# Kernel tuning notes

Measured on AMD Instinct MI355X. Metric: run time of the kernel, lower is better.

Reference implementation:

```python
import jax, jax.numpy as jnp
import numpy as np

K = 7          # involution kernel size
GC = 16        # group_channels (hardcoded in module)
BN_EPS = 1e-5
LN_EPS = 1e-6


def _forward(x, conv1_w, conv1_b, bn_gamma, bn_beta, bn_mean, bn_var,
             conv2_w, conv2_b, ln_w, ln_b, w1, b1, w2, b2):
    b, c, h, w = x.shape
    groups = c // GC
    # --- involution: dynamic kernel generation (1x1 conv -> BN(eval) -> ReLU -> 1x1 conv) ---
    t = jnp.einsum('bchw,oc->bohw', x, conv1_w) + conv1_b[None, :, None, None]
    t = (t - bn_mean[None, :, None, None]) * (bn_gamma / jnp.sqrt(bn_var + BN_EPS))[None, :, None, None] \
        + bn_beta[None, :, None, None]
    t = jax.nn.relu(t)
    wgt = jnp.einsum('bchw,oc->bohw', t, conv2_w) + conv2_b[None, :, None, None]
    wgt = wgt.reshape(b, groups, K * K, h, w)                  # (b,g,k2,h,w)
    # --- unfold: gather kxk neighborhoods (channel-major, then kh, kw — matches torch Unfold) ---
    p = (K - 1) // 2
    xp = jnp.pad(x, ((0, 0), (0, 0), (p, p), (p, p)))
    patches = jnp.stack([xp[:, :, i:i + h, j:j + w]
                         for i in range(K) for j in range(K)], axis=2)   # (b,c,k2,h,w)
    patches = patches.reshape(b, groups, GC, K * K, h, w)
    # weighted sum over kernel positions
    out = jnp.einsum('bgkhw,bgckhw->bgchw', wgt, patches).reshape(b, c, h, w)
    # --- LN + MLP residual (channels_last) ---
    y = out.transpose(0, 2, 3, 1)                               # (b,h,w,c)
    mu = y.mean(-1, keepdims=True)
    var = ((y - mu) ** 2).mean(-1, keepdims=True)
    y = (y - mu) / jnp.sqrt(var + LN_EPS) * ln_w + ln_b
    y = jax.nn.gelu(y @ w1.T + b1, approximate=False)           # torch GELU = exact erf
    y = y @ w2.T + b2                                           # dropout_rate=0 -> identity
    return y.transpose(0, 3, 1, 2) + x


def setup_inputs() -> dict:
    key = jax.random.key(0)
    ks = jax.random.split(key, 6)
    dim = 128
    groups = dim // GC
    red = dim // 4
    b, h, w = 8, 56, 56
    return {
        'x': jax.random.normal(ks[0], (b, dim, h, w), jnp.float32),
        'conv1_w': jax.random.normal(ks[1], (red, dim), jnp.float32) * (1.0 / np.sqrt(dim)),
        'conv1_b': jnp.zeros((red,), jnp.float32),
        'bn_gamma': jnp.ones((red,), jnp.float32),
        'bn_beta': jnp.zeros((red,), jnp.float32),
        'bn_mean': jnp.zeros((red,), jnp.float32),
        'bn_var': jnp.ones((red,), jnp.float32),
        'conv2_w': jax.random.normal(ks[2], (K * K * groups, red), jnp.float32) * (1.0 / np.sqrt(red)),
        'conv2_b': jnp.zeros((K * K * groups,), jnp.float32),
        'ln_w': jnp.ones((dim,), jnp.float32),
        'ln_b': jnp.zeros((dim,), jnp.float32),
        'w1': jax.random.normal(ks[3], (4 * dim, dim), jnp.float32) * (1.0 / np.sqrt(dim)),
        'b1': jnp.zeros((4 * dim,), jnp.float32),
        'w2': jax.random.normal(ks[4], (dim, 4 * dim), jnp.float32) * (1.0 / np.sqrt(4 * dim)),
        'b2': jnp.zeros((dim,), jnp.float32),
    }


def reference(x, conv1_w, conv1_b, bn_gamma, bn_beta, bn_mean, bn_var,
              conv2_w, conv2_b, ln_w, ln_b, w1, b1, w2, b2):
    return _forward(x, conv1_w, conv1_b, bn_gamma, bn_beta, bn_mean, bn_var,
                    conv2_w, conv2_b, ln_w, ln_b, w1, b1, w2, b2)
```

## Files before the change

### kernel.cpp

```cpp
#include <hip/hip_runtime.h>
#include <hip/hip_bf16.h>
#include <math.h>

#define HW    3136
#define WIMG  56
#define NPIX  25088
#define CIN   128
#define RED   32
#define NGROUP 8
#define GCH   16
#define KKK   49

typedef __attribute__((ext_vector_type(8))) short short8;
typedef __attribute__((ext_vector_type(4))) float f32x4;
typedef unsigned short ushort_t;

static __device__ __forceinline__ unsigned int f2b(float f) {
    union { __hip_bfloat16 b; unsigned short u; } cv;
    cv.b = __float2bfloat16(f);
    return (unsigned int)cv.u;
}

static __device__ __forceinline__ float gelu_t(float h) {
    float z = h * fmaf(0.0356774081f, h * h, 0.7978845608f);
    float e = __expf(-2.f * z);
    return __fdividef(h, 1.f + e);
}

__global__ __launch_bounds__(256) void k_prep(const float* __restrict__ conv1_w,
    const float* __restrict__ conv1_b, const float* __restrict__ bn_g,
    const float* __restrict__ bn_b, const float* __restrict__ bn_m,
    const float* __restrict__ bn_v, const float* __restrict__ conv2_w,
    const float* __restrict__ ln_w, const float* __restrict__ w1,
    const float* __restrict__ w2,
    ushort_t* __restrict__ c1b, ushort_t* __restrict__ c2b,
    ushort_t* __restrict__ lw1b, ushort_t* __restrict__ w2b,
    float* __restrict__ sc1, float* __restrict__ sh1)
{
    int id = blockIdx.x * 256 + threadIdx.x;
    w2b[id] = (ushort_t)f2b(w2[id]);
    int c = id & 127;
    lw1b[id] = (ushort_t)f2b(w1[id] * ln_w[c]);
    if (id < 4096)  c1b[id] = (ushort_t)f2b(conv1_w[id]);
    if (id < 12800) c2b[id] = (id < 12544) ? (ushort_t)f2b(conv2_w[id]) : (ushort_t)0;
    if (id < 32) {
        float sc = bn_g[id] * rsqrtf(bn_v[id] + 1e-5f);
        sc1[id] = sc;
        sh1[id] = (conv1_b[id] - bn_m[id]) * sc + bn_b[id];
    }
}

__global__ void k_prep2(const float* __restrict__ w1, const float* __restrict__ ln_w,
    const float* __restrict__ ln_b, const float* __restrict__ b1,
    float* __restrict__ s1, float* __restrict__ t1)
{
    int n = threadIdx.x;
    const float* wr = w1 + (size_t)n * 128;
    float s = 0.f, t = 0.f;
    #pragma unroll 8
    for (int c = 0; c < 128; ++c) { float w = wr[c]; s += ln_w[c] * w; t += ln_b[c] * w; }
    s1[n] = s; t1[n] = t + b1[n];
}

__global__ __launch_bounds__(256) void k_mega(const float* __restrict__ x,
    const short* __restrict__ c1b, const short* __restrict__ c2b,
    const float* __restrict__ sc1, const float* __restrict__ sh1,
    const float* __restrict__ c2bias,
    const ushort_t* __restrict__ lw1b, const ushort_t* __restrict__ w2b,
    const float* __restrict__ s1, const float* __restrict__ t1,
    const float* __restrict__ b2, float* __restrict__ outp)
{
    __shared__ __align__(16) char smem[79936];
    short* swg  = (short*)smem;
    short* sh   = (short*)smem;
    short* sx   = (short*)smem + 26656;
    short* st   = (short*)(smem + 70720);
    float* sred  = (float*)(smem + 70720);
    float* sred2 = sred + 1088;
    float* smu   = sred2 + 1088;
    float* srs   = smu + 64;

    int tid  = threadIdx.x;
    int P0   = blockIdx.x * 64;
    int b    = P0 / HW;
    int p0i  = P0 - b * HW;
    int lane = tid & 63, wv = tid >> 6;
    int ln15 = lane & 15, quad = lane >> 4;

    const float* xb = x + (size_t)b * CIN * HW + p0i;
    #pragma unroll
    for (int it = 0; it < 32; ++it) {
        int idx = it * 256 + tid;
        int c = idx >> 6, pp = idx & 63;
        sx[pp * 136 + c] = (short)f2b(xb[(size_t)c * HW + pp]);
    }
    __syncthreads();

    f32x4 acc1c[2] = {(f32x4)0.f, (f32x4)0.f};
    #pragma unroll
    for (int kc = 0; kc < 128; kc += 32) {
        short8 af = *(const short8*)&sx[(wv * 16 + ln15) * 136 + kc + quad * 8];
        #pragma unroll
        for (int nt = 0; nt < 2; ++nt) {
            short8 bf = *(const short8*)&c1b[(size_t)(nt * 16 + ln15) * 128 + kc + quad * 8];
            acc1c[nt] = __builtin_amdgcn_mfma_f32_16x16x32_bf16(af, bf, acc1c[nt], 0, 0, 0);
        }
    }
    #pragma unroll
    for (int nt = 0; nt < 2; ++nt) {
        int o = nt * 16 + ln15;
        float sc = sc1[o], shv = sh1[o];
        #pragma unroll
        for (int r = 0; r < 4; ++r) {
            float tv = fmaxf(acc1c[nt][r] * sc + shv, 0.f);
            st[(wv * 16 + quad * 4 + r) * 40 + o] = (short)f2b(tv);
        }
    }
    short8 af2 = *(const short8*)&st[(wv * 16 + ln15) * 40 + quad * 8];
    f32x4 zc = (f32x4)0.f;
    #pragma unroll
    for (int nt = 0; nt < 25; ++nt) {
        int gk = nt * 16 + ln15;
        short8 bf2 = *(const short8*)&c2b[(size_t)gk * 32 + quad * 8];
        f32x4 a2 = __builtin_amdgcn_mfma_f32_16x16x32_bf16(af2, bf2, zc, 0, 0, 0);
        if (gk < 392) {
            float bj = c2bias[gk];
            uint2 pk;
            pk.x = f2b(a2[0] + bj) | (f2b(a2[1] + bj) << 16);
            pk.y = f2b(a2[2] + bj) | (f2b(a2[3] + bj) << 16);
            *(uint2*)&swg[gk * 68 + wv * 16 + quad * 4] = pk;
        }
    }
    __syncthreads();

    {
        int q   = tid & 15;
        int gy  = tid >> 4;
        int g   = gy >> 1;
        int sub = gy & 1;
        int pl0 = q * 4;
        int p   = p0i + pl0;
        int prow = p / WIMG;
        int pcol = p - prow * WIMG;
        const float* xc = x + ((size_t)b * CIN + g * GCH + sub * 8) * HW;
        float acc[4][8];
        #pragma unroll
        for (int i = 0; i < 4; ++i)
            #pragma unroll
            for (int c = 0; c < 8; ++c) acc[i][c] = 0.f;
        bool c_lo = (pcol >= 4);
        bool c_hi = (pcol <= 48);
        #pragma unroll
        for (int dy = -3; dy <= 3; ++dy) {
            int grow = prow + dy;
            if (grow < 0 || grow >= WIMG) continue;
            float wkf[7][4];
            #pragma unroll
            for (int dx = 0; dx < 7; ++dx) {
                int gk = g * KKK + (dy + 3) * 7 + dx;
                uint2 wld = *(const uint2*)&swg[gk * 68 + pl0];
                wkf[dx][0] = __uint_as_float(wld.x << 16);
                wkf[dx][1] = __uint_as_float(wld.x & 0xffff0000u);
                wkf[dx][2] = __uint_as_float(wld.y << 16);
                wkf[dx][3] = __uint_as_float(wld.y & 0xffff0000u);
            }
            const float* xrow = xc + grow * WIMG + pcol;
            #pragma unroll
            for (int c = 0; c < 8; ++c) {
                const float* xr = xrow + (size_t)c * HW;
                float4 v0 = c_lo ? *(const float4*)(xr - 4) : make_float4(0.f,0.f,0.f,0.f);
                float4 v1 = *(const float4*)(xr);
                float4 v2 = c_hi ? *(const float4*)(xr + 4) : make_float4(0.f,0.f,0.f,0.f);
                float vv[12] = {v0.x,v0.y,v0.z,v0.w, v1.x,v1.y,v1.z,v1.w, v2.x,v2.y,v2.z,v2.w};
                #pragma unroll
                for (int dx = 0; dx < 7; ++dx)
                    #pragma unroll
                    for (int i = 0; i < 4; ++i)
                        acc[i][c] += wkf[dx][i] * vv[i + dx + 1];
            }
        }
        #pragma unroll
        for (int i = 0; i < 4; ++i) {
            unsigned pk[4];
            float s = 0.f, s2 = 0.f;
            #pragma unroll
            for (int h = 0; h < 4; ++h)
                pk[h] = f2b(acc[i][2*h]) | (f2b(acc[i][2*h+1]) << 16);
            #pragma unroll
            for (int c = 0; c < 8; ++c) { s += acc[i][c]; s2 += acc[i][c] * acc[i][c]; }
            *(uint4*)&sx[(pl0 + i) * 136 + g * 16 + sub * 8] = make_uint4(pk[0],pk[1],pk[2],pk[3]);
            sred [(pl0 + i) * 17 + gy] = s;
            sred2[(pl0 + i) * 17 + gy] = s2;
        }
    }
    __syncthreads();

    if (tid < 64) {
        float s = 0.f, s2 = 0.f;
        #pragma unroll
        for (int gy = 0; gy < 16; ++gy) { s += sred[tid * 17 + gy]; s2 += sred2[tid * 17 + gy]; }
        float m = s * (1.f / 128.f);
        float v = s2 * (1.f / 128.f) - m * m;
        smu[tid] = m;
        srs[tid] = rsqrtf(v + 1e-6f);
    }
    __syncthreads();

    float mu_r[4], rs_r[4];
    #pragma unroll
    for (int tn = 0; tn < 4; ++tn) {
        int px = tn * 16 + ln15;
        mu_r[tn] = smu[px];
        rs_r[tn] = srs[px];
    }

    f32x4 acc2[4][2];
    #pragma unroll
    for (int i = 0; i < 4; ++i)
        #pragma unroll
        for (int j = 0; j < 2; ++j) acc2[i][j] = (f32x4)0.f;

    for (int j = 0; j < 4; ++j) {
        f32x4 acc1[2][4];
        #pragma unroll
        for (int tm = 0; tm < 2; ++tm)
            #pragma unroll
            for (int tn = 0; tn < 4; ++tn) acc1[tm][tn] = (f32x4)0.f;
        #pragma unroll
        for (int kc = 0; kc < 128; kc += 32) {
            short8 af[2], bf[4];
            #pragma unroll
            for (int tm = 0; tm < 2; ++tm)
                af[tm] = *(const short8*)&lw1b[(size_t)(j * 128 + wv * 32 + tm * 16 + ln15) * 128 + kc + quad * 8];
            #pragma unroll
            for (int tn = 0; tn < 4; ++tn)
                bf[tn] = *(const short8*)&sx[(tn * 16 + ln15) * 136 + kc + quad * 8];
            #pragma unroll
            for (int tm = 0; tm < 2; ++tm)
                #pragma unroll
                for (int tn = 0; tn < 4; ++tn)
                    acc1[tm][tn] = __builtin_amdgcn_mfma_f32_16x16x32_bf16(af[tm], bf[tn], acc1[tm][tn], 0, 0, 0);
        }
        #pragma unroll
        for (int tm = 0; tm < 2; ++tm) {
            int nl = wv * 32 + tm * 16 + quad * 4;
            int n  = j * 128 + nl;
            float4 s14 = *(const float4*)&s1[n];
            float4 t14 = *(const float4*)&t1[n];
            #pragma unroll
            for (int tn = 0; tn < 4; ++tn) {
                int px = tn * 16 + ln15;
                float g0 = gelu_t(rs_r[tn] * (acc1[tm][tn][0] - mu_r[tn] * s14.x) + t14.x);
                float g1 = gelu_t(rs_r[tn] * (acc1[tm][tn][1] - mu_r[tn] * s14.y) + t14.y);
                float g2 = gelu_t(rs_r[tn] * (acc1[tm][tn][2] - mu_r[tn] * s14.z) + t14.z);
                float g3 = gelu_t(rs_r[tn] * (acc1[tm][tn][3] - mu_r[tn] * s14.w) + t14.w);
                uint2 pk;
                pk.x = f2b(g0) | (f2b(g1) << 16);
                pk.y = f2b(g2) | (f2b(g3) << 16);
                *(uint2*)&sh[px * 136 + nl] = pk;
            }
        }
        __syncthreads();
        #pragma unroll
        for (int kc = 0; kc < 128; kc += 32) {
            short8 af[4], bf[2];
            #pragma unroll
            for (int tm = 0; tm < 4; ++tm)
                af[tm] = *(const short8*)&sh[(tm * 16 + ln15) * 136 + kc + quad * 8];
            #pragma unroll
            for (int tn = 0; tn < 2; ++tn)
                bf[tn] = *(const short8*)&w2b[(size_t)(wv * 32 + tn * 16 + ln15) * 512 + j * 128 + kc + quad * 8];
            #pragma unroll
            for (int tm = 0; tm < 4; ++tm)
                #pragma unroll
                for (int tn = 0; tn < 2; ++tn)
                    acc2[tm][tn] = __builtin_amdgcn_mfma_f32_16x16x32_bf16(af[tm], bf[tn], acc2[tm][tn], 0, 0, 0);
        }
        __syncthreads();
    }

    #pragma unroll
    for (int tm = 0; tm < 4; ++tm) {
        int p = p0i + tm * 16 + quad * 4;
        #pragma unroll
        for (int tn = 0; tn < 2; ++tn) {
            int c = wv * 32 + tn * 16 + ln15;
            size_t base = ((size_t)b * CIN + c) * HW + p;
            float bj = b2[c];
            float4 rv = *(const float4*)&x[base];
            float4 ov = make_float4(acc2[tm][tn][0] + bj + rv.x,
                                    acc2[tm][tn][1] + bj + rv.y,
                                    acc2[tm][tn][2] + bj + rv.z,
                                    acc2[tm][tn][3] + bj + rv.w);
            *(float4*)&outp[base] = ov;
        }
    }
}

extern "C" void kernel_launch(void* const* d_in, const int* in_sizes, int n_in,
                              void* d_out, int out_size, void* d_ws, size_t ws_size,
                              hipStream_t stream) {
    const float* x       = (const float*)d_in[0];
    const float* conv1_w = (const float*)d_in[1];
    const float* conv1_b = (const float*)d_in[2];
    const float* bn_g    = (const float*)d_in[3];
    const float* bn_b    = (const float*)d_in[4];
    const float* bn_m    = (const float*)d_in[5];
    const float* bn_v    = (const float*)d_in[6];
    const float* conv2_w = (const float*)d_in[7];
    const float* conv2_b = (const float*)d_in[8];
    const float* ln_w    = (const float*)d_in[9];
    const float* ln_b    = (const float*)d_in[10];
    const float* w1      = (const float*)d_in[11];
    const float* b1      = (const float*)d_in[12];
    const float* w2      = (const float*)d_in[13];
    const float* b2      = (const float*)d_in[14];
    float* out = (float*)d_out;

    float* F = (float*)d_ws;
    float* sc1  = F;
    float* sh1  = F + 32;
    float* s1   = F + 64;
    float* t1   = F + 576;
    ushort_t* S    = (ushort_t*)(F + 1088);
    ushort_t* c1b  = S;
    ushort_t* c2b  = c1b + 4096;
    ushort_t* lw1b = c2b + 12800;
    ushort_t* w2b  = lw1b + 65536;

    k_prep <<<256, 256, 0, stream>>>(conv1_w, conv1_b, bn_g, bn_b, bn_m, bn_v,
                                     conv2_w, ln_w, w1, w2, c1b, c2b, lw1b, w2b, sc1, sh1);
    k_prep2<<<1, 512, 0, stream>>>(w1, ln_w, ln_b, b1, s1, t1);
    k_mega <<<392, 256, 0, stream>>>(x, (const short*)c1b, (const short*)c2b,
                                     sc1, sh1, conv2_b, lw1b, w2b, s1, t1, b2, out);
}
```

Measured before the change: 149.9 us.

## Halve pixel tile per block to 32 and double grid for occupancy

Shrinks the per-block pixel tile from 64 to 32 and launches 784 blocks instead of 392. Shared memory drops from about 80KB to about 45KB, so more blocks fit per CU and there are more blocks than the 256 CUs. The intent is better latency hiding and fuller use of the CUs. Work is redistributed across the four waves: the first GEMM splits by M/N tile, the kernel-generation GEMM strides over N tiles, and involution threads now handle 4 channels each. The cost is that every block reloads the MLP weights (lw1b, w2b) for half as many pixels, doubling weight traffic from L2.

```diff
diff --git a/kernel.cpp b/kernel.cpp
--- a/kernel.cpp
+++ b/kernel.cpp
@@ -10,6 +10,7 @@
 #define NGROUP 8
 #define GCH   16
 #define KKK   49
+#define TP    32
 
 typedef __attribute__((ext_vector_type(8))) short short8;
 typedef __attribute__((ext_vector_type(4))) float f32x4;
@@ -70,18 +71,18 @@
     const float* __restrict__ s1, const float* __restrict__ t1,
     const float* __restrict__ b2, float* __restrict__ outp)
 {
-    __shared__ __align__(16) char smem[79936];
+    __shared__ __align__(16) char smem[44608];
     short* swg  = (short*)smem;
     short* sh   = (short*)smem;
-    short* sx   = (short*)smem + 26656;
-    short* st   = (short*)(smem + 70720);
-    float* sred  = (float*)(smem + 70720);
-    float* sred2 = sred + 1088;
-    float* smu   = sred2 + 1088;
-    float* srs   = smu + 64;
+    short* sx   = (short*)(smem + 27200);
+    short* st   = (short*)(smem + 35904);
+    float* sred  = (float*)(smem + 35904);
+    float* sred2 = sred + 1056;
+    float* smu   = sred2 + 1056;
+    float* srs   = smu + 32;
 
     int tid  = threadIdx.x;
-    int P0   = blockIdx.x * 64;
+    int P0   = blockIdx.x * TP;
     int b    = P0 / HW;
     int p0i  = P0 - b * HW;
     int lane = tid & 63, wv = tid >> 6;
@@ -89,65 +90,69 @@
 
     const float* xb = x + (size_t)b * CIN * HW + p0i;
     #pragma unroll
-    for (int it = 0; it < 32; ++it) {
+    for (int it = 0; it < 16; ++it) {
         int idx = it * 256 + tid;
-        int c = idx >> 6, pp = idx & 63;
+        int c = idx >> 5, pp = idx & 31;
         sx[pp * 136 + c] = (short)f2b(xb[(size_t)c * HW + pp]);
     }
     __syncthreads();
 
-    f32x4 acc1c[2] = {(f32x4)0.f, (f32x4)0.f};
-    #pragma unroll
-    for (int kc = 0; kc < 128; kc += 32) {
-        short8 af = *(const short8*)&sx[(wv * 16 + ln15) * 136 + kc + quad * 8];
-        #pragma unroll
-        for (int nt = 0; nt < 2; ++nt) {
+    {
+        int mt = wv & 1, nt = wv >> 1;
+        f32x4 a1 = (f32x4)0.f;
+        #pragma unroll
+        for (int kc = 0; kc < 128; kc += 32) {
+            short8 af = *(const short8*)&sx[(mt * 16 + ln15) * 136 + kc + quad * 8];
             short8 bf = *(const short8*)&c1b[(size_t)(nt * 16 + ln15) * 128 + kc + quad * 8];
-            acc1c[nt] = __builtin_amdgcn_mfma_f32_16x16x32_bf16(af, bf, acc1c[nt], 0, 0, 0);
-        }
-    }
-    #pragma unroll
-    for (int nt = 0; nt < 2; ++nt) {
+            a1 = __builtin_amdgcn_mfma_f32_16x16x32_bf16(af, bf, a1, 0, 0, 0);
+        }
         int o = nt * 16 + ln15;
         float sc = sc1[o], shv = sh1[o];
         #pragma unroll
         for (int r = 0; r < 4; ++r) {
-            float tv = fmaxf(acc1c[nt][r] * sc + shv, 0.f);
-            st[(wv * 16 + quad * 4 + r) * 40 + o] = (short)f2b(tv);
-        }
-    }
-    short8 af2 = *(const short8*)&st[(wv * 16 + ln15) * 40 + quad * 8];
-    f32x4 zc = (f32x4)0.f;
-    #pragma unroll
-    for (int nt = 0; nt < 25; ++nt) {
-        int gk = nt * 16 + ln15;
-        short8 bf2 = *(const short8*)&c2b[(size_t)gk * 32 + quad * 8];
-        f32x4 a2 = __builtin_amdgcn_mfma_f32_16x16x32_bf16(af2, bf2, zc, 0, 0, 0);
-        if (gk < 392) {
-            float bj = c2bias[gk];
-            uint2 pk;
-            pk.x = f2b(a2[0] + bj) | (f2b(a2[1] + bj) << 16);
-            pk.y = f2b(a2[2] + bj) | (f2b(a2[3] + bj) << 16);
-            *(uint2*)&swg[gk * 68 + wv * 16 + quad * 4] = pk;
+            float tv = fmaxf(a1[r] * sc + shv, 0.f);
+            st[(mt * 16 + quad * 4 + r) * 40 + o] = (short)f2b(tv);
         }
     }
     __syncthreads();
 
     {
-        int q   = tid & 15;
-        int gy  = tid >> 4;
-        int g   = gy >> 1;
-        int sub = gy & 1;
+        short8 af2[2];
+        #pragma unroll
+        for (int mt = 0; mt < 2; ++mt)
+            af2[mt] = *(const short8*)&st[(mt * 16 + ln15) * 40 + quad * 8];
+        f32x4 zc = (f32x4)0.f;
+        for (int nt = wv; nt < 25; nt += 4) {
+            int gk = nt * 16 + ln15;
+            short8 bf2 = *(const short8*)&c2b[(size_t)gk * 32 + quad * 8];
+            float bj = (gk < 392) ? c2bias[gk] : 0.f;
+            #pragma unroll
+            for (int mt = 0; mt < 2; ++mt) {
+                f32x4 a2 = __builtin_amdgcn_mfma_f32_16x16x32_bf16(af2[mt], bf2, zc, 0, 0, 0);
+                uint2 pk;
+                pk.x = f2b(a2[0] + bj) | (f2b(a2[1] + bj) << 16);
+                pk.y = f2b(a2[2] + bj) | (f2b(a2[3] + bj) << 16);
+                *(uint2*)&swg[gk * 34 + mt * 16 + quad * 4] = pk;
+            }
+        }
+    }
+    __syncthreads();
+
+    {
+        int q   = tid & 7;
+        int gy  = tid >> 3;
+        int g   = gy >> 2;
+        int sub = gy & 3;
         int pl0 = q * 4;
         int p   = p0i + pl0;
         int prow = p / WIMG;
         int pcol = p - prow * WIMG;
-        const float* xc = x + ((size_t)b * CIN + g * GCH + sub * 8) * HW;
-        float acc[4][8];
+        const float* xc = x + ((size_t)b * CIN + g * GCH + sub * 4) * HW;
+        float acc[4][4];
         #pragma unroll
         for (int i = 0; i < 4; ++i)
             #pragma unroll
-            for (int c = 0; c < 8; ++c) acc[i][c] = 0.f;
+            for (int c = 0; c < 4; ++c) acc[i][c] = 0.f;
         bool c_lo = (pcol >= 4);
         bool c_hi = (pcol <= 48);
         #pragma unroll
@@ -158,7 +163,7 @@
             #pragma unroll
             for (int dx = 0; dx < 7; ++dx) {
                 int gk = g * KKK + (dy + 3) * 7 + dx;
-                uint2 wld = *(const uint2*)&swg[gk * 68 + pl0];
+                uint2 wld = *(const uint2*)&swg[gk * 34 + pl0];
                 wkf[dx][0] = __uint_as_float(wld.x << 16);
                 wkf[dx][1] = __uint_as_float(wld.x & 0xffff0000u);
                 wkf[dx][2] = __uint_as_float(wld.y << 16);
@@ -166,7 +171,7 @@
             }
             const float* xrow = xc + grow * WIMG + pcol;
             #pragma unroll
-            for (int c = 0; c < 8; ++c) {
+            for (int c = 0; c < 4; ++c) {
                 const float* xr = xrow + (size_t)c * HW;
                 float4 v0 = c_lo ? *(const float4*)(xr - 4) : make_float4(0.f,0.f,0.f,0.f);
                 float4 v1 = *(const float4*)(xr);
@@ -181,24 +186,23 @@
         }
         #pragma unroll
         for (int i = 0; i < 4; ++i) {
-            unsigned pk[4];
             float s = 0.f, s2 = 0.f;
             #pragma unroll
-            for (int h = 0; h < 4; ++h)
-                pk[h] = f2b(acc[i][2*h]) | (f2b(acc[i][2*h+1]) << 16);
-            #pragma unroll
-            for (int c = 0; c < 8; ++c) { s += acc[i][c]; s2 += acc[i][c] * acc[i][c]; }
-            *(uint4*)&sx[(pl0 + i) * 136 + g * 16 + sub * 8] = make_uint4(pk[0],pk[1],pk[2],pk[3]);
-            sred [(pl0 + i) * 17 + gy] = s;
-            sred2[(pl0 + i) * 17 + gy] = s2;
-        }
-    }
-    __syncthreads();
-
-    if (tid < 64) {
+            for (int c = 0; c < 4; ++c) { s += acc[i][c]; s2 += acc[i][c] * acc[i][c]; }
+            uint2 pk;
+            pk.x = f2b(acc[i][0]) | (f2b(acc[i][1]) << 16);
+            pk.y = f2b(acc[i][2]) | (f2b(acc[i][3]) << 16);
+            *(uint2*)&sx[(pl0 + i) * 136 + g * GCH + sub * 4] = pk;
+            sred [(pl0 + i) * 33 + gy] = s;
+            sred2[(pl0 + i) * 33 + gy] = s2;
+        }
+    }
+    __syncthreads();
+
+    if (tid < TP) {
         float s = 0.f, s2 = 0.f;
         #pragma unroll
-        for (int gy = 0; gy < 16; ++gy) { s += sred[tid * 17 + gy]; s2 += sred2[tid * 17 + gy]; }
+        for (int gy = 0; gy < 32; ++gy) { s += sred[tid * 33 + gy]; s2 += sred2[tid * 33 + gy]; }
         float m = s * (1.f / 128.f);
         float v = s2 * (1.f / 128.f) - m * m;
         smu[tid] = m;
@@ -206,39 +210,39 @@
     }
     __syncthreads();
 
-    float mu_r[4], rs_r[4];
+    float mu_r[2], rs_r[2];
     #pragma unroll
-    for (int tn = 0; tn < 4; ++tn) {
+    for (int tn = 0; tn < 2; ++tn) {
         int px = tn * 16 + ln15;
         mu_r[tn] = smu[px];
         rs_r[tn] = srs[px];
     }
 
-    f32x4 acc2[4][2];
+    f32x4 acc2[2][2];
     #pragma unroll
-    for (int i = 0; i < 4; ++i)
+    for (int i = 0; i < 2; ++i)
         #pragma unroll
         for (int j = 0; j < 2; ++j) acc2[i][j] = (f32x4)0.f;
 
     for (int j = 0; j < 4; ++j) {
-        f32x4 acc1[2][4];
+        f32x4 acc1[2][2];
         #pragma unroll
         for (int tm = 0; tm < 2; ++tm)
             #pragma unroll
-            for (int tn = 0; tn < 4; ++tn) acc1[tm][tn] = (f32x4)0.f;
+            for (int tn = 0; tn < 2; ++tn) acc1[tm][tn] = (f32x4)0.f;
         #pragma unroll
         for (int kc = 0; kc < 128; kc += 32) {
-            short8 af[2], bf[4];
+            short8 af[2], bf[2];
             #pragma unroll
             for (int tm = 0; tm < 2; ++tm)
                 af[tm] = *(const short8*)&lw1b[(size_t)(j * 128 + wv * 32 + tm * 16 + ln15) * 128 + kc + quad * 8];
             #pragma unroll
-            for (int tn = 0; tn < 4; ++tn)
+            for (int tn = 0; tn < 2; ++tn)
                 bf[tn] = *(const short8*)&sx[(tn * 16 + ln15) * 136 + kc + quad * 8];
             #pragma unroll
             for (int tm = 0; tm < 2; ++tm)
                 #pragma unroll
-                for (int tn = 0; tn < 4; ++tn)
+                for (int tn = 0; tn < 2; ++tn)
                     acc1[tm][tn] = __builtin_amdgcn_mfma_f32_16x16x32_bf16(af[tm], bf[tn], acc1[tm][tn], 0, 0, 0);
         }
         #pragma unroll
@@ -248,7 +252,7 @@
             float4 s14 = *(const float4*)&s1[n];
             float4 t14 = *(const float4*)&t1[n];
             #pragma unroll
-            for (int tn = 0; tn < 4; ++tn) {
+            for (int tn = 0; tn < 2; ++tn) {
                 int px = tn * 16 + ln15;
                 float g0 = gelu_t(rs_r[tn] * (acc1[tm][tn][0] - mu_r[tn] * s14.x) + t14.x);
                 float g1 = gelu_t(rs_r[tn] * (acc1[tm][tn][1] - mu_r[tn] * s14.y) + t14.y);
@@ -263,15 +267,15 @@
         __syncthreads();
         #pragma unroll
         for (int kc = 0; kc < 128; kc += 32) {
-            short8 af[4], bf[2];
-            #pragma unroll
-            for (int tm = 0; tm < 4; ++tm)
+            short8 af[2], bf[2];
+            #pragma unroll
+            for (int tm = 0; tm < 2; ++tm)
                 af[tm] = *(const short8*)&sh[(tm * 16 + ln15) * 136 + kc + quad * 8];
             #pragma unroll
             for (int tn = 0; tn < 2; ++tn)
                 bf[tn] = *(const short8*)&w2b[(size_t)(wv * 32 + tn * 16 + ln15) * 512 + j * 128 + kc + quad * 8];
             #pragma unroll
-            for (int tm = 0; tm < 4; ++tm)
+            for (int tm = 0; tm < 2; ++tm)
                 #pragma unroll
                 for (int tn = 0; tn < 2; ++tn)
                     acc2[tm][tn] = __builtin_amdgcn_mfma_f32_16x16x32_bf16(af[tm], bf[tn], acc2[tm][tn], 0, 0, 0);
@@ -280,7 +284,7 @@
     }
 
     #pragma unroll
-    for (int tm = 0; tm < 4; ++tm) {
+    for (int tm = 0; tm < 2; ++tm) {
         int p = p0i + tm * 16 + quad * 4;
         #pragma unroll
         for (int tn = 0; tn < 2; ++tn) {
@@ -331,6 +335,6 @@
     k_prep <<<256, 256, 0, stream>>>(conv1_w, conv1_b, bn_g, bn_b, bn_m, bn_v,
                                      conv2_w, ln_w, w1, w2, c1b, c2b, lw1b, w2b, sc1, sh1);
     k_prep2<<<1, 512, 0, stream>>>(w1, ln_w, ln_b, b1, s1, t1);
-    k_mega <<<392, 256, 0, stream>>>(x, (const short*)c1b, (const short*)c2b,
+    k_mega <<<784, 256, 0, stream>>>(x, (const short*)c1b, (const short*)c2b,
                                      sc1, sh1, conv2_b, lw1b, w2b, s1, t1, b2, out);
 }
```

Result: slower. 173.8 us (+15.9%).

## Split MLP stage by pixel rows per wave to drop block barriers

Applied to the files above, without the earlier changes.

Restructures the fused LN+MLP stage so each wave owns 16 pixels and computes all hidden and output channels for them, instead of splitting channels across waves over 64 shared pixels. Each wave stages its GELU hidden activations in a private shared-memory slice, which removes the two __syncthreads per hidden chunk. In exchange, every wave now streams the full w1 and w2 weight rows from global/L2 rather than a quarter of them, raising weight load traffic per block.

```diff
diff --git a/kernel.cpp b/kernel.cpp
--- a/kernel.cpp
+++ b/kernel.cpp
@@ -72,7 +72,6 @@
 {
     __shared__ __align__(16) char smem[79936];
     short* swg  = (short*)smem;
-    short* sh   = (short*)smem;
     short* sx   = (short*)smem + 26656;
     short* st   = (short*)(smem + 70720);
     float* sred  = (float*)(smem + 70720);
@@ -206,92 +205,65 @@
     }
     __syncthreads();
 
-    float mu_r[4], rs_r[4];
-    #pragma unroll
-    for (int tn = 0; tn < 4; ++tn) {
-        int px = tn * 16 + ln15;
-        mu_r[tn] = smu[px];
-        rs_r[tn] = srs[px];
-    }
-
-    f32x4 acc2[4][2];
-    #pragma unroll
-    for (int i = 0; i < 4; ++i)
-        #pragma unroll
-        for (int j = 0; j < 2; ++j) acc2[i][j] = (f32x4)0.f;
+    float mu_l = smu[wv * 16 + ln15];
+    float rs_l = srs[wv * 16 + ln15];
+
+    short* hwv = (short*)smem + wv * 2176;
+
+    f32x4 acc2[8];
+    #pragma unroll
+    for (int i = 0; i < 8; ++i) acc2[i] = (f32x4)0.f;
 
     for (int j = 0; j < 4; ++j) {
-        f32x4 acc1[2][4];
-        #pragma unroll
-        for (int tm = 0; tm < 2; ++tm)
-            #pragma unroll
-            for (int tn = 0; tn < 4; ++tn) acc1[tm][tn] = (f32x4)0.f;
+        f32x4 acc1[8];
+        #pragma unroll
+        for (int i = 0; i < 8; ++i) acc1[i] = (f32x4)0.f;
         #pragma unroll
         for (int kc = 0; kc < 128; kc += 32) {
-            short8 af[2], bf[4];
-            #pragma unroll
-            for (int tm = 0; tm < 2; ++tm)
-                af[tm] = *(const short8*)&lw1b[(size_t)(j * 128 + wv * 32 + tm * 16 + ln15) * 128 + kc + quad * 8];
-            #pragma unroll
-            for (int tn = 0; tn < 4; ++tn)
-                bf[tn] = *(const short8*)&sx[(tn * 16 + ln15) * 136 + kc + quad * 8];
-            #pragma unroll
-            for (int tm = 0; tm < 2; ++tm)
-                #pragma unroll
-                for (int tn = 0; tn < 4; ++tn)
-                    acc1[tm][tn] = __builtin_amdgcn_mfma_f32_16x16x32_bf16(af[tm], bf[tn], acc1[tm][tn], 0, 0, 0);
-        }
-        #pragma unroll
-        for (int tm = 0; tm < 2; ++tm) {
-            int nl = wv * 32 + tm * 16 + quad * 4;
-            int n  = j * 128 + nl;
+            short8 bf = *(const short8*)&sx[(wv * 16 + ln15) * 136 + kc + quad * 8];
+            #pragma unroll
+            for (int mt = 0; mt < 8; ++mt) {
+                short8 af = *(const short8*)&lw1b[(size_t)(j * 128 + mt * 16 + ln15) * 128 + kc + quad * 8];
+                acc1[mt] = __builtin_amdgcn_mfma_f32_16x16x32_bf16(af, bf, acc1[mt], 0, 0, 0);
+            }
+        }
+        #pragma unroll
+        for (int mt = 0; mt < 8; ++mt) {
+            int n = j * 128 + mt * 16 + quad * 4;
             float4 s14 = *(const float4*)&s1[n];
             float4 t14 = *(const float4*)&t1[n];
-            #pragma unroll
-            for (int tn = 0; tn < 4; ++tn) {
-                int px = tn * 16 + ln15;
-                float g0 = gelu_t(rs_r[tn] * (acc1[tm][tn][0] - mu_r[tn] * s14.x) + t14.x);
-                float g1 = gelu_t(rs_r[tn] * (acc1[tm][tn][1] - mu_r[tn] * s14.y) + t14.y);
-                float g2 = gelu_t(rs_r[tn] * (acc1[tm][tn][2] - mu_r[tn] * s14.z) + t14.z);
-                float g3 = gelu_t(rs_r[tn] * (acc1[tm][tn][3] - mu_r[tn] * s14.w) + t14.w);
-                uint2 pk;
-                pk.x = f2b(g0) | (f2b(g1) << 16);
-                pk.y = f2b(g2) | (f2b(g3) << 16);
-                *(uint2*)&sh[px * 136 + nl] = pk;
+            float g0 = gelu_t(rs_l * (acc1[mt][0] - mu_l * s14.x) + t14.x);
+            float g1 = gelu_t(rs_l * (acc1[mt][1] - mu_l * s14.y) + t14.y);
+            float g2 = gelu_t(rs_l * (acc1[mt][2] - mu_l * s14.z) + t14.z);
+            float g3 = gelu_t(rs_l * (acc1[mt][3] - mu_l * s14.w) + t14.w);
+            uint2 pk;
+            pk.x = f2b(g0) | (f2b(g1) << 16);
+            pk.y = f2b(g2) | (f2b(g3) << 16);
+            *(uint2*)&hwv[ln15 * 136 + mt * 16 + quad * 4] = pk;
+        }
+        #pragma unroll
+        for (int kc = 0; kc < 128; kc += 32) {
+            short8 af = *(const short8*)&hwv[ln15 * 136 + kc + quad * 8];
+            #pragma unroll
+            for (int ct = 0; ct < 8; ++ct) {
+                short8 bf = *(const short8*)&w2b[(size_t)(ct * 16 + ln15) * 512 + j * 128 + kc + quad * 8];
+                acc2[ct] = __builtin_amdgcn_mfma_f32_16x16x32_bf16(af, bf, acc2[ct], 0, 0, 0);
             }
         }
-        __syncthreads();
-        #pragma unroll
-        for (int kc = 0; kc < 128; kc += 32) {
-            short8 af[4], bf[2];
-            #pragma unroll
-            for (int tm = 0; tm < 4; ++tm)
-                af[tm] = *(const short8*)&sh[(tm * 16 + ln15) * 136 + kc + quad * 8];
-            #pragma unroll
-            for (int tn = 0; tn < 2; ++tn)
-                bf[tn] = *(const short8*)&w2b[(size_t)(wv * 32 + tn * 16 + ln15) * 512 + j * 128 + kc + quad * 8];
-            #pragma unroll
-            for (int tm = 0; tm < 4; ++tm)
-                #pragma unroll
-                for (int tn = 0; tn < 2; ++tn)
-                    acc2[tm][tn] = __builtin_amdgcn_mfma_f32_16x16x32_bf16(af[tm], bf[tn], acc2[tm][tn], 0, 0, 0);
-        }
-        __syncthreads();
-    }
-
-    #pragma unroll
-    for (int tm = 0; tm < 4; ++tm) {
-        int p = p0i + tm * 16 + quad * 4;
-        #pragma unroll
-        for (int tn = 0; tn < 2; ++tn) {
-            int c = wv * 32 + tn * 16 + ln15;
-            size_t base = ((size_t)b * CIN + c) * HW + p;
+    }
+
+    {
+        int pw = p0i + wv * 16 + quad * 4;
+        #pragma unroll
+        for (int ct = 0; ct < 8; ++ct) {
+            int c = ct * 16 + ln15;
+            size_t base = ((size_t)b * CIN + c) * HW + pw;
             float bj = b2[c];
             float4 rv = *(const float4*)&x[base];
-            float4 ov = make_float4(acc2[tm][tn][0] + bj + rv.x,
-                                    acc2[tm][tn][1] + bj + rv.y,
-                                    acc2[tm][tn][2] + bj + rv.z,
-                                    acc2[tm][tn][3] + bj + rv.w);
+            float4 ov = make_float4(acc2[ct][0] + bj + rv.x,
+                                    acc2[ct][1] + bj + rv.y,
+                                    acc2[ct][2] + bj + rv.z,
+                                    acc2[ct][3] + bj + rv.w);
             *(float4*)&outp[base] = ov;
         }
     }
```

After: 187.4 us. +25.0%, slower.

## Prefetch MLP weight fragments, drop LN reduction sync, remap blocks across batches

Applied to the files above, without the earlier changes.

Block indices are remapped so consecutive blocks belong to different images, which spreads L2/HBM access across the batch. The separate LayerNorm statistics pass and its barrier are removed: every lane now reduces the per-pixel partial sums itself with float4 LDS reads on a padded stride. Both MLP weight matrices' fragments for each j-chunk are loaded up front into registers, so global loads overlap the MFMA work. The cost is higher register pressure, which may lower occupancy, plus slightly more LDS.

```diff
diff --git a/kernel.cpp b/kernel.cpp
--- a/kernel.cpp
+++ b/kernel.cpp
@@ -70,18 +70,18 @@
     const float* __restrict__ s1, const float* __restrict__ t1,
     const float* __restrict__ b2, float* __restrict__ outp)
 {
-    __shared__ __align__(16) char smem[79936];
+    __shared__ __align__(16) char smem[80960];
     short* swg  = (short*)smem;
     short* sh   = (short*)smem;
     short* sx   = (short*)smem + 26656;
     short* st   = (short*)(smem + 70720);
     float* sred  = (float*)(smem + 70720);
-    float* sred2 = sred + 1088;
-    float* smu   = sred2 + 1088;
-    float* srs   = smu + 64;
+    float* sred2 = sred + 1280;
 
     int tid  = threadIdx.x;
-    int P0   = blockIdx.x * 64;
+    int bid  = blockIdx.x;
+    int sblk = (bid & 7) * 49 + (bid >> 3);
+    int P0   = sblk * 64;
     int b    = P0 / HW;
     int p0i  = P0 - b * HW;
     int lane = tid & 63, wv = tid >> 6;
@@ -189,20 +189,9 @@
             #pragma unroll
             for (int c = 0; c < 8; ++c) { s += acc[i][c]; s2 += acc[i][c] * acc[i][c]; }
             *(uint4*)&sx[(pl0 + i) * 136 + g * 16 + sub * 8] = make_uint4(pk[0],pk[1],pk[2],pk[3]);
-            sred [(pl0 + i) * 17 + gy] = s;
-            sred2[(pl0 + i) * 17 + gy] = s2;
-        }
-    }
-    __syncthreads();
-
-    if (tid < 64) {
-        float s = 0.f, s2 = 0.f;
-        #pragma unroll
-        for (int gy = 0; gy < 16; ++gy) { s += sred[tid * 17 + gy]; s2 += sred2[tid * 17 + gy]; }
-        float m = s * (1.f / 128.f);
-        float v = s2 * (1.f / 128.f) - m * m;
-        smu[tid] = m;
-        srs[tid] = rsqrtf(v + 1e-6f);
+            sred [(pl0 + i) * 20 + gy] = s;
+            sred2[(pl0 + i) * 20 + gy] = s2;
+        }
     }
     __syncthreads();
 
@@ -210,8 +199,17 @@
     #pragma unroll
     for (int tn = 0; tn < 4; ++tn) {
         int px = tn * 16 + ln15;
-        mu_r[tn] = smu[px];
-        rs_r[tn] = srs[px];
+        float s = 0.f, s2 = 0.f;
+        #pragma unroll
+        for (int k4 = 0; k4 < 4; ++k4) {
+            float4 a = *(const float4*)&sred [px * 20 + k4 * 4];
+            float4 c = *(const float4*)&sred2[px * 20 + k4 * 4];
+            s  += a.x + a.y + a.z + a.w;
+            s2 += c.x + c.y + c.z + c.w;
+        }
+        float m = s * (1.f / 128.f);
+        mu_r[tn] = m;
+        rs_r[tn] = rsqrtf(s2 * (1.f / 128.f) - m * m + 1e-6f);
     }
 
     f32x4 acc2[4][2];
@@ -221,25 +219,32 @@
         for (int j = 0; j < 2; ++j) acc2[i][j] = (f32x4)0.f;
 
     for (int j = 0; j < 4; ++j) {
+        short8 a1f[4][2], b2f[4][2];
+        #pragma unroll
+        for (int k4 = 0; k4 < 4; ++k4) {
+            #pragma unroll
+            for (int tm = 0; tm < 2; ++tm)
+                a1f[k4][tm] = *(const short8*)&lw1b[(size_t)(j * 128 + wv * 32 + tm * 16 + ln15) * 128 + k4 * 32 + quad * 8];
+            #pragma unroll
+            for (int tn = 0; tn < 2; ++tn)
+                b2f[k4][tn] = *(const short8*)&w2b[(size_t)(wv * 32 + tn * 16 + ln15) * 512 + j * 128 + k4 * 32 + quad * 8];
+        }
         f32x4 acc1[2][4];
         #pragma unroll
         for (int tm = 0; tm < 2; ++tm)
             #pragma unroll
             for (int tn = 0; tn < 4; ++tn) acc1[tm][tn] = (f32x4)0.f;
         #pragma unroll
-        for (int kc = 0; kc < 128; kc += 32) {
-            short8 af[2], bf[4];
-            #pragma unroll
-            for (int tm = 0; tm < 2; ++tm)
-                af[tm] = *(const short8*)&lw1b[(size_t)(j * 128 + wv * 32 + tm * 16 + ln15) * 128 + kc + quad * 8];
+        for (int k4 = 0; k4 < 4; ++k4) {
+            short8 bf[4];
             #pragma unroll
             for (int tn = 0; tn < 4; ++tn)
-                bf[tn] = *(const short8*)&sx[(tn * 16 + ln15) * 136 + kc + quad * 8];
+                bf[tn] = *(const short8*)&sx[(tn * 16 + ln15) * 136 + k4 * 32 + quad * 8];
             #pragma unroll
             for (int tm = 0; tm < 2; ++tm)
                 #pragma unroll
                 for (int tn = 0; tn < 4; ++tn)
-                    acc1[tm][tn] = __builtin_amdgcn_mfma_f32_16x16x32_bf16(af[tm], bf[tn], acc1[tm][tn], 0, 0, 0);
+                    acc1[tm][tn] = __builtin_amdgcn_mfma_f32_16x16x32_bf16(a1f[k4][tm], bf[tn], acc1[tm][tn], 0, 0, 0);
         }
         #pragma unroll
         for (int tm = 0; tm < 2; ++tm) {
@@ -262,19 +267,16 @@
         }
         __syncthreads();
         #pragma unroll
-        for (int kc = 0; kc < 128; kc += 32) {
-            short8 af[4], bf[2];
+        for (int k4 = 0; k4 < 4; ++k4) {
+            short8 af[4];
             #pragma unroll
             for (int tm = 0; tm < 4; ++tm)
-                af[tm] = *(const short8*)&sh[(tm * 16 + ln15) * 136 + kc + quad * 8];
-            #pragma unroll
-            for (int tn = 0; tn < 2; ++tn)
-                bf[tn] = *(const short8*)&w2b[(size_t)(wv * 32 + tn * 16 + ln15) * 512 + j * 128 + kc + quad * 8];
+                af[tm] = *(const short8*)&sh[(tm * 16 + ln15) * 136 + k4 * 32 + quad * 8];
             #pragma unroll
             for (int tm = 0; tm < 4; ++tm)
                 #pragma unroll
                 for (int tn = 0; tn < 2; ++tn)
-                    acc2[tm][tn] = __builtin_amdgcn_mfma_f32_16x16x32_bf16(af[tm], bf[tn], acc2[tm][tn], 0, 0, 0);
+                    acc2[tm][tn] = __builtin_amdgcn_mfma_f32_16x16x32_bf16(af[tm], b2f[k4][tn], acc2[tm][tn], 0, 0, 0);
         }
         __syncthreads();
     }
```

New measurement: 153.3 us. +2.2%, slower.
